# Kernel optimization log

Measured on AMD Instinct MI355X. Metric: run time of the kernel, lower is better.

The kernel has to match this reference:

```python
import jax, jax.numpy as jnp
import numpy as np

MAX_ITER = 3
DAMPING = 1e-3
HUBER_B = 0.02
LAMBDA_ICP, LAMBDA_RGB = 1.0, 1e-6
DIST_THRESH = 0.1


def pixel_grid(H, W):
    j, i = jnp.meshgrid(jnp.arange(H, dtype=jnp.float32), jnp.arange(W, dtype=jnp.float32), indexing='ij')
    return i, j  # i = x (col), j = y (row)


def compute_vertex(depth, K):
    fx, fy, cx, cy = K[0, 0], K[1, 1], K[0, 2], K[1, 2]
    H, W = depth.shape
    i, j = pixel_grid(H, W)
    return jnp.stack([(i - cx) / fx, (j - cy) / fy, jnp.ones_like(i)], -1) * depth[..., None]


def sobel(img, normalize=True):
    # replicate-padded 3x3 Sobel cross-correlation, img [H,W,C]
    p = jnp.pad(img, ((1, 1), (1, 1), (0, 0)), mode='edge')
    dx = (p[:-2, 2:] - p[:-2, :-2]) + 2.0 * (p[1:-1, 2:] - p[1:-1, :-2]) + (p[2:, 2:] - p[2:, :-2])
    dy = (p[2:, :-2] - p[:-2, :-2]) + 2.0 * (p[2:, 1:-1] - p[:-2, 1:-1]) + (p[2:, 2:] - p[:-2, 2:])
    if normalize:
        mag = jnp.sqrt(dx * dx + dy * dy + 1e-8)
        dx, dy = dx / mag, dy / mag
    return dx, dy


def compute_normal(vmap_):
    dx, dy = sobel(vmap_, normalize=False)
    n = jnp.cross(dx, dy)
    n = n / (jnp.linalg.norm(n, axis=-1, keepdims=True) + 1e-8)
    d = vmap_[..., 2]
    invalid = (d <= d.min()) | (d >= d.max())
    return jnp.where(invalid[..., None], 0.0, n)


def warp_jacobian(depth, K):
    fx, fy, cx, cy = K[0, 0], K[1, 1], K[0, 2], K[1, 2]
    H, W = depth.shape
    i, j = pixel_grid(H, W)
    x = (i - cx) / fx * depth
    y = (j - cy) / fy * depth
    invD = 1.0 / depth
    invD2 = invD * invD
    xy = x * y
    O = jnp.zeros_like(depth)
    dx_dp = jnp.stack([-invD2 * xy, 1.0 + x * x * invD2, -y * invD, invD, O, -invD2 * x], -1)
    dy_dp = jnp.stack([-1.0 - invD2 * y * y, xy * invD2, x * invD, O, invD, -invD2 * y], -1)
    return dx_dp * fx, dy_dp * fy


def bilinear(feat, u, v):
    # grid_sample(mode=bilinear, padding=border, align_corners=True) on pixel coords
    H, W, _ = feat.shape
    u = jnp.clip(u, 0.0, W - 1.0)
    v = jnp.clip(v, 0.0, H - 1.0)
    u0 = jnp.floor(u)
    v0 = jnp.floor(v)
    wu = (u - u0)[..., None]
    wv = (v - v0)[..., None]
    u0i = u0.astype(jnp.int32)
    v0i = v0.astype(jnp.int32)
    u1i = jnp.minimum(u0i + 1, W - 1)
    v1i = jnp.minimum(v0i + 1, H - 1)
    f00 = feat[v0i, u0i]
    f01 = feat[v0i, u1i]
    f10 = feat[v1i, u0i]
    f11 = feat[v1i, u1i]
    return (f00 * (1 - wu) + f01 * wu) * (1 - wv) + (f10 * (1 - wu) + f11 * wu) * wv


def project(vt, K, H, W):
    z = vt[..., 2]
    u = vt[..., 0] / z * K[0, 0] + K[0, 2]
    v = vt[..., 1] / z * K[1, 1] + K[1, 2]
    inview = (u > 0) & (u < W - 1) & (v > 0) & (v < H - 1) & (z > 0)
    return u, v, inview


def huber_weight(x, b=HUBER_B):
    rho = jnp.where(x <= b, x * x, 2.0 * b * x - b * b)
    x_safe = jnp.where(x < 1e-8, 1.0, x)
    return jnp.sqrt(rho + 1e-16) / x_safe


def skew(w):
    z = jnp.zeros((), w.dtype)
    return jnp.stack([jnp.stack([z, -w[2], w[1]]), jnp.stack([w[2], z, -w[0]]), jnp.stack([-w[1], w[0], z])])


def exp_so3(w):
    Wh = skew(w)
    th2 = jnp.maximum(jnp.sum(w * w), 1e-30)
    th = jnp.sqrt(th2)
    R = jnp.eye(3, dtype=w.dtype) + Wh * (jnp.sin(th) / th) + (Wh @ Wh) * ((1.0 - jnp.cos(th)) / th2)
    return jnp.where(th <= 1e-10, jnp.eye(3, dtype=w.dtype), R)


def icp_residuals(vertex0, vertex1, normal1, mask0, pose, K):
    H, W, _ = vertex0.shape
    R, t = pose[:3, :3], pose[:3, 3]
    v0t = vertex0 @ R.T + t  # [H,W,3]
    u, v, inview = project(v0t, K, H, W)
    v1w = bilinear(vertex1, u, v)
    n1w = bilinear(normal1, u, v)
    diff = v0t - v1w
    valid = inview & mask0 & (v1w[..., 2] > 0) & (jnp.linalg.norm(diff, axis=-1) < DIST_THRESH)
    res = jnp.where(valid, jnp.sum(n1w * diff, -1), 0.0)  # point-to-plane
    J = jnp.where(valid[..., None], jnp.concatenate([jnp.cross(v0t, n1w), n1w], -1), 0.0)  # [H,W,6]
    w = huber_weight(jnp.abs(res))
    return (w * res).reshape(-1, 1), (w[..., None] * J).reshape(-1, 1, 6)


def rgb_residuals(pose, vertex0, x0, x1, K, mask0):
    H, W, _ = x0.shape
    R, t = pose[:3, :3], pose[:3, 3]
    v0t = vertex0 @ R.T + t
    u, v, inview = project(v0t, K, H, W)
    x1w = bilinear(x1, u, v)
    invalid = (~inview) | (~mask0)
    res = jnp.where(invalid[..., None], 0.0, x1w - x0)
    return res, invalid


def inverse_update_pose(Hm, Rhs, pose):
    xi = (jnp.linalg.inv(Hm) @ Rhs).reshape(-1)
    dR = exp_so3(-xi[:3])
    dt = -dR @ xi[3:]
    R1 = dR @ pose[:3, :3]
    t1 = dR @ pose[:3, 3] + dt
    top = jnp.concatenate([R1, t1[:, None]], 1)
    return jnp.concatenate([top, pose[3:4, :]], 0)


def color_icp(pose10, depth0, depth1, x0, x1, K):
    H, W, C = x0.shape
    vertex0 = compute_vertex(depth0, K)
    normal0 = compute_normal(vertex0)  # computed as in original
    mask0 = depth0 > 0.0
    vertex1 = compute_vertex(depth1, K)
    normal1 = compute_normal(vertex1)
    # pre-computable inverse-compositional RGB jacobian: normalized image grads x warp jacobian
    gx, gy = sobel(x0, normalize=True)  # [H,W,C]
    Jx, Jy = warp_jacobian(depth0, K)  # [H,W,6]
    J_rgb_pre = gx[..., None] * Jx[:, :, None, :] + gy[..., None] * Jy[:, :, None, :]  # [H,W,C,6]
    pose = pose10
    for _ in range(MAX_ITER):
        r_icp, J_icp = icp_residuals(vertex0, vertex1, normal1, mask0, pose, K)
        JtWJ = LAMBDA_ICP * jnp.einsum('nci,ncj->ij', J_icp, J_icp)
        JtR = LAMBDA_ICP * jnp.einsum('nci,nc->i', J_icp, r_icp)
        r_rgb, invalid = rgb_residuals(pose, vertex0, x0, x1, K, mask0)
        J_rgb = jnp.where(invalid[..., None, None], 0.0, J_rgb_pre).reshape(-1, C, 6)
        JtWJ = JtWJ + LAMBDA_RGB * jnp.einsum('nci,ncj->ij', J_rgb, J_rgb)
        JtR = JtR + LAMBDA_RGB * jnp.einsum('nci,nc->i', J_rgb, r_rgb.reshape(-1, C))
        Hm = JtWJ + jnp.eye(6) * (jnp.trace(JtWJ) * DAMPING)  # Levenberg-Marquardt damping
        pose = inverse_update_pose(Hm, JtR.reshape(6, 1), pose)
    return pose


def setup_inputs() -> dict:
    key = jax.random.key(0)
    k = jax.random.split(key, 6)
    H, W = 960, 1280
    depth0 = 0.5 + 2.5 * jax.random.uniform(k[0], (H, W), jnp.float32)
    depth1 = 0.5 + 2.5 * jax.random.uniform(k[1], (H, W), jnp.float32)
    x0 = jax.random.uniform(k[2], (H, W, 3), jnp.float32)
    x1 = jax.random.uniform(k[3], (H, W, 3), jnp.float32)
    K = jnp.array([[1050.0, 0.0, (W - 1) / 2.0], [0.0, 1050.0, (H - 1) / 2.0], [0.0, 0.0, 1.0]], jnp.float32)
    w = 0.01 * jax.random.normal(k[4], (3,), jnp.float32)
    t = 0.01 * jax.random.normal(k[5], (3,), jnp.float32)
    R = exp_so3(w)
    pose10 = jnp.concatenate([jnp.concatenate([R, t[:, None]], 1),
                              jnp.array([[0.0, 0.0, 0.0, 1.0]], jnp.float32)], 0)
    return {'pose10': pose10, 'depth0': depth0, 'depth1': depth1, 'x0': x0, 'x1': x1, 'K': K}


def reference(pose10, depth0, depth1, x0, x1, K):
    return color_icp(pose10, depth0, depth1, x0, x1, K)
```

## Files before the change

kernel.cpp:

```cpp
#include <hip/hip_runtime.h>
#include <math.h>

#define HH 960
#define WW 1280
#define NPIX (HH*WW)
#define BPR (WW/256)
#define NBLK_ROW (NPIX/256)
#define NBLK_MAIN (NPIX/(256*2))
#define MM_BLOCKS 512
#define TW 258
#define PSTRIDE 28

#define WS_POSE_OFF    0
#define WS_BMIN_OFF    128
#define WS_BMAX_OFF    2176
#define WS_PARTIAL_OFF 4352
#define WS_NX_OFF      273152

__device__ __forceinline__ int clampi(int v, int lo, int hi){ return v<lo?lo:(v>hi?hi:v); }

__global__ __launch_bounds__(256) void k_pre1(const float* __restrict__ depth1,
                                              const float* __restrict__ pose_in,
                                              float* __restrict__ pose,
                                              float* __restrict__ bmin,
                                              float* __restrict__ bmax){
  int t = threadIdx.x;
  if (blockIdx.x == 0 && t < 16) pose[t] = pose_in[t];
  float mn = INFINITY, mx = 0.f;
  for (int i = blockIdx.x*256 + t; i < NPIX; i += MM_BLOCKS*256){
    float d = depth1[i];
    mn = fminf(mn, d); mx = fmaxf(mx, d);
  }
  #pragma unroll
  for (int off = 32; off; off >>= 1){
    mn = fminf(mn, __shfl_down(mn, off));
    mx = fmaxf(mx, __shfl_down(mx, off));
  }
  __shared__ float smn[4], smx[4];
  int lane = t & 63, wid = t >> 6;
  if (lane == 0){ smn[wid] = mn; smx[wid] = mx; }
  __syncthreads();
  if (t == 0){
    bmin[blockIdx.x] = fminf(fminf(smn[0], smn[1]), fminf(smn[2], smn[3]));
    bmax[blockIdx.x] = fmaxf(fmaxf(smx[0], smx[1]), fmaxf(smx[2], smx[3]));
  }
}

__global__ __launch_bounds__(256) void k_pre2(const float* __restrict__ depth1,
                                              const float* __restrict__ x1,
                                              const float* __restrict__ Kd,
                                              const float* __restrict__ bmin,
                                              const float* __restrict__ bmax,
                                              float* __restrict__ nx1){
  int t = threadIdx.x;
  float mn = fminf(bmin[t], bmin[t+256]);
  float mx = fmaxf(bmax[t], bmax[t+256]);
  #pragma unroll
  for (int off = 32; off; off >>= 1){
    mn = fminf(mn, __shfl_down(mn, off));
    mx = fmaxf(mx, __shfl_down(mx, off));
  }
  __shared__ float smn[4], smx[4];
  __shared__ float sdmn, sdmx;
  int lane = t & 63, wid = t >> 6;
  if (lane == 0){ smn[wid] = mn; smx[wid] = mx; }
  __syncthreads();
  if (t == 0){
    sdmn = fminf(fminf(smn[0], smn[1]), fminf(smn[2], smn[3]));
    sdmx = fmaxf(fmaxf(smx[0], smx[1]), fmaxf(smx[2], smx[3]));
  }
  __syncthreads();
  float dmn = sdmn, dmx = sdmx;

  int bid = blockIdx.x;
  int py = bid / BPR;
  int px = (bid % BPR)*256 + t;
  float fx = Kd[0], fy = Kd[4], cx = Kd[2], cy = Kd[5];
  float invfx = 1.f/fx, invfy = 1.f/fy;
  float vx[3][3], vy[3][3], vz[3][3];
  #pragma unroll
  for (int dr = 0; dr < 3; dr++){
    int r = clampi(py + dr - 1, 0, HH-1);
    #pragma unroll
    for (int dc = 0; dc < 3; dc++){
      int c = clampi(px + dc - 1, 0, WW-1);
      float d = depth1[r*WW + c];
      vx[dr][dc] = ((float)c - cx)*invfx*d;
      vy[dr][dc] = ((float)r - cy)*invfy*d;
      vz[dr][dc] = d;
    }
  }
  float ax_ = (vx[0][2]-vx[0][0]) + 2.f*(vx[1][2]-vx[1][0]) + (vx[2][2]-vx[2][0]);
  float ay_ = (vy[0][2]-vy[0][0]) + 2.f*(vy[1][2]-vy[1][0]) + (vy[2][2]-vy[2][0]);
  float az_ = (vz[0][2]-vz[0][0]) + 2.f*(vz[1][2]-vz[1][0]) + (vz[2][2]-vz[2][0]);
  float bx_ = (vx[2][0]-vx[0][0]) + 2.f*(vx[2][1]-vx[0][1]) + (vx[2][2]-vx[0][2]);
  float by_ = (vy[2][0]-vy[0][0]) + 2.f*(vy[2][1]-vy[0][1]) + (vy[2][2]-vy[0][2]);
  float bz_ = (vz[2][0]-vz[0][0]) + 2.f*(vz[2][1]-vz[0][1]) + (vz[2][2]-vz[0][2]);
  float nx = ay_*bz_ - az_*by_;
  float ny = az_*bx_ - ax_*bz_;
  float nz = ax_*by_ - ay_*bx_;
  float nrm = sqrtf(nx*nx + ny*ny + nz*nz) + 1e-8f;
  float rn  = __builtin_amdgcn_rcpf(nrm);
  nx *= rn; ny *= rn; nz *= rn;
  float dcen = vz[1][1];
  if (dcen <= dmn || dcen >= dmx){ nx = 0.f; ny = 0.f; nz = 0.f; }
  int idx = py*WW + px;
  const float* q = &x1[idx*3];
  float4 a; a.x = nx;   a.y = ny;   a.z = nz;   a.w = dcen;
  float4 b; b.x = q[0]; b.y = q[1]; b.z = q[2]; b.w = 0.f;
  ((float4*)nx1)[idx*2+0] = a;
  ((float4*)nx1)[idx*2+1] = b;
}

__global__ __launch_bounds__(256) void k_main(const float* __restrict__ depth0,
                                              const float* __restrict__ x0,
                                              const float* __restrict__ nx1,
                                              const float* __restrict__ Kd,
                                              const float* __restrict__ pose,
                                              float* __restrict__ partial){
  int t = threadIdx.x;
  int bid = (blockIdx.x & 7)*(NBLK_MAIN/8) + (blockIdx.x >> 3);
  int pr = bid / BPR;
  int cs = bid % BPR;
  int py0 = pr*2;
  int colbase = cs*256 - 1;
  int px = cs*256 + t;

  __shared__ float tile[4*TW*3];
  for (int s = t; s < 4*TW; s += 256){
    int r = s / TW, c = s - r*TW;
    int gr = clampi(py0 - 1 + r, 0, HH-1);
    int gc = clampi(colbase + c, 0, WW-1);
    const float* q = &x0[(gr*WW + gc)*3];
    tile[s*3+0] = q[0]; tile[s*3+1] = q[1]; tile[s*3+2] = q[2];
  }

  int idx0 = py0*WW + px;
  float d0a = depth0[idx0];
  float d0b = depth0[idx0 + WW];
  __syncthreads();

  float fx = Kd[0], fy = Kd[4], cx = Kd[2], cy = Kd[5];
  float inv_fx = 1.f/fx, inv_fy = 1.f/fy;
  float R00=pose[0], R01=pose[1], R02=pose[2],  tx=pose[3];
  float R10=pose[4], R11=pose[5], R12=pose[6],  ty=pose[7];
  float R20=pose[8], R21=pose[9], R22=pose[10], tz=pose[11];

  float acc[27];
  #pragma unroll
  for (int k = 0; k < 27; k++) acc[k] = 0.f;

  const float4* nx4 = (const float4*)nx1;

  #pragma unroll
  for (int kp = 0; kp < 2; kp++){
    int py = py0 + kp;

    float d0 = (kp == 0) ? d0a : d0b;
    bool m0 = d0 > 0.f;
    float v0x = ((float)px - cx)*inv_fx*d0;
    float v0y = ((float)py - cy)*inv_fy*d0;
    float v0z = d0;
    float X = R00*v0x + R01*v0y + R02*v0z + tx;
    float Y = R10*v0x + R11*v0y + R12*v0z + ty;
    float Z = R20*v0x + R21*v0y + R22*v0z + tz;
    float invZ = __builtin_amdgcn_rcpf(Z);
    invZ = invZ*(2.0f - Z*invZ);
    float u = X*invZ*fx + cx;
    float v = Y*invZ*fy + cy;
    bool inview = (u > 0.f) && (u < (float)(WW-1)) && (v > 0.f) && (v < (float)(HH-1)) && (Z > 0.f);

    float uc = fminf(fmaxf(u, 0.f), (float)(WW-1));
    float vc = fminf(fmaxf(v, 0.f), (float)(HH-1));
    float u0f = floorf(uc), v0f = floorf(vc);
    float wu = uc - u0f, wv = vc - v0f;
    int u0i = clampi((int)u0f, 0, WW-1);
    int v0i = clampi((int)v0f, 0, HH-1);
    int u1i = min(u0i + 1, WW-1);
    int v1i = min(v0i + 1, HH-1);
    int i00 = v0i*WW + u0i, i01 = v0i*WW + u1i, i10 = v1i*WW + u0i, i11 = v1i*WW + u1i;
    float w00 = (1.f-wu)*(1.f-wv), w01 = wu*(1.f-wv), w10 = (1.f-wu)*wv, w11 = wu*wv;

    float4 n00 = nx4[i00*2], c00 = nx4[i00*2+1];
    float4 n01 = nx4[i01*2], c01 = nx4[i01*2+1];
    float4 n10 = nx4[i10*2], c10 = nx4[i10*2+1];
    float4 n11 = nx4[i11*2], c11 = nx4[i11*2+1];

    float t0 = w00*n00.w, t1 = w01*n01.w, t2 = w10*n10.w, t3 = w11*n11.w;
    float u0c = ((float)u0i - cx)*inv_fx, u1c = ((float)u1i - cx)*inv_fx;
    float v0c = ((float)v0i - cy)*inv_fy, v1c = ((float)v1i - cy)*inv_fy;
    float s2 = (t0+t1)+(t2+t3);
    float s0 = u0c*(t0+t2) + u1c*(t1+t3);
    float s1 = v0c*(t0+t1) + v1c*(t2+t3);
    float nx = n00.x*w00 + n01.x*w01 + n10.x*w10 + n11.x*w11;
    float ny = n00.y*w00 + n01.y*w01 + n10.y*w10 + n11.y*w11;
    float nz = n00.z*w00 + n01.z*w01 + n10.z*w10 + n11.z*w11;

    float dfx = X - s0, dfy = Y - s1, dfz = Z - s2;
    bool valid = inview && m0 && (s2 > 0.f) && (dfx*dfx + dfy*dfy + dfz*dfz < 0.01f);
    float res = 0.f;
    float J[6] = {0.f,0.f,0.f,0.f,0.f,0.f};
    if (valid){
      res = nx*dfx + ny*dfy + nz*dfz;
      J[0] = Y*nz - Z*ny;
      J[1] = Z*nx - X*nz;
      J[2] = X*ny - Y*nx;
      J[3] = nx; J[4] = ny; J[5] = nz;
    }
    float axv = fabsf(res);
    float rho = (axv <= 0.02f) ? axv*axv : (0.04f*axv - 0.0004f);
    float xs  = (axv < 1e-8f) ? 1.f : axv;
    float hw  = sqrtf(rho + 1e-16f) * __builtin_amdgcn_rcpf(xs);
    float wr  = hw*res;
    float wJ[6];
    #pragma unroll
    for (int i = 0; i < 6; i++) wJ[i] = hw*J[i];
    {
      int k = 0;
      #pragma unroll
      for (int i = 0; i < 6; i++)
        #pragma unroll
        for (int j = i; j < 6; j++)
          acc[k++] += wJ[i]*wJ[j];
      #pragma unroll
      for (int i = 0; i < 6; i++) acc[21+i] += wJ[i]*wr;
    }

    if (inview && m0){
      float xw[3];
      xw[0] = c00.x*w00 + c01.x*w01 + c10.x*w10 + c11.x*w11;
      xw[1] = c00.y*w00 + c01.y*w01 + c10.y*w10 + c11.y*w11;
      xw[2] = c00.z*w00 + c01.z*w01 + c10.z*w10 + c11.z*w11;

      float ga = 0.f, gb = 0.f, gc2 = 0.f, rx = 0.f, ry = 0.f;
      #pragma unroll
      for (int ch = 0; ch < 3; ch++){
        float p00 = tile[((kp+0)*TW + (t+0))*3 + ch];
        float p01 = tile[((kp+0)*TW + (t+1))*3 + ch];
        float p02 = tile[((kp+0)*TW + (t+2))*3 + ch];
        float p10 = tile[((kp+1)*TW + (t+0))*3 + ch];
        float p11 = tile[((kp+1)*TW + (t+1))*3 + ch];
        float p12 = tile[((kp+1)*TW + (t+2))*3 + ch];
        float p20 = tile[((kp+2)*TW + (t+0))*3 + ch];
        float p21 = tile[((kp+2)*TW + (t+1))*3 + ch];
        float p22 = tile[((kp+2)*TW + (t+2))*3 + ch];
        float dx = (p02-p00) + 2.f*(p12-p10) + (p22-p20);
        float dy = (p20-p00) + 2.f*(p21-p01) + (p22-p02);
        float rinv = __builtin_amdgcn_rsqf(dx*dx + dy*dy + 1e-8f);
        float gx = dx*rinv, gy = dy*rinv;
        float rr = xw[ch] - p11;
        ga  += gx*gx; gb += gx*gy; gc2 += gy*gy;
        rx  += gx*rr; ry += gy*rr;
      }
      ga *= 1e-6f; gb *= 1e-6f; gc2 *= 1e-6f; rx *= 1e-6f; ry *= 1e-6f;

      float invD = __builtin_amdgcn_rcpf(d0), invD2 = invD*invD;
      float xy = v0x*v0y;
      float Jx[6] = { fx*(-invD2*xy), fx*(1.f + v0x*v0x*invD2), fx*(-v0y*invD), fx*invD, 0.f, fx*(-invD2*v0x) };
      float Jy[6] = { fy*(-1.f - invD2*v0y*v0y), fy*(xy*invD2), fy*(v0x*invD), 0.f, fy*invD, fy*(-invD2*v0y) };
      float P[6], Q[6];
      #pragma unroll
      for (int i = 0; i < 6; i++){ P[i] = ga*Jx[i] + gb*Jy[i]; Q[i] = gb*Jx[i] + gc2*Jy[i]; }
      int k = 0;
      #pragma unroll
      for (int i = 0; i < 6; i++)
        #pragma unroll
        for (int j = i; j < 6; j++)
          acc[k++] += Jx[j]*P[i] + Jy[j]*Q[i];
      #pragma unroll
      for (int i = 0; i < 6; i++) acc[21+i] += Jx[i]*rx + Jy[i]*ry;
    }
  }

  __shared__ float lds[108];
  int lane = t & 63;
  int wid  = t >> 6;
  #pragma unroll
  for (int k = 0; k < 27; k++){
    float vv = acc[k];
    vv += __shfl_down(vv, 32); vv += __shfl_down(vv, 16); vv += __shfl_down(vv, 8);
    vv += __shfl_down(vv, 4);  vv += __shfl_down(vv, 2);  vv += __shfl_down(vv, 1);
    if (lane == 0) lds[wid*27 + k] = vv;
  }
  __syncthreads();
  if (t < 27)
    partial[bid*PSTRIDE + t] = lds[t] + lds[27+t] + lds[54+t] + lds[81+t];
  else if (t == 27)
    partial[bid*PSTRIDE + 27] = 0.f;
}

__global__ __launch_bounds__(256) void k_solve(const float* __restrict__ partial,
                                               float* __restrict__ pose,
                                               float* __restrict__ outp){
  int t = threadIdx.x;
  double acc[PSTRIDE];
  #pragma unroll
  for (int k = 0; k < PSTRIDE; k++) acc[k] = 0.0;
  const float4* p4 = (const float4*)partial;
  for (int r = t; r < NBLK_MAIN; r += 256){
    #pragma unroll
    for (int q = 0; q < 7; q++){
      float4 vv = p4[r*7 + q];
      acc[q*4+0] += (double)vv.x;
      acc[q*4+1] += (double)vv.y;
      acc[q*4+2] += (double)vv.z;
      acc[q*4+3] += (double)vv.w;
    }
  }
  __shared__ double lds[4*PSTRIDE];
  int lane = t & 63, wid = t >> 6;
  #pragma unroll
  for (int k = 0; k < PSTRIDE; k++){
    double vv = acc[k];
    vv += __shfl_down(vv, 32); vv += __shfl_down(vv, 16); vv += __shfl_down(vv, 8);
    vv += __shfl_down(vv, 4);  vv += __shfl_down(vv, 2);  vv += __shfl_down(vv, 1);
    if (lane == 0) lds[wid*PSTRIDE + k] = vv;
  }
  __syncthreads();
  if (t == 0){
    double s[PSTRIDE];
    #pragma unroll
    for (int k = 0; k < PSTRIDE; k++)
      s[k] = lds[k] + lds[PSTRIDE+k] + lds[2*PSTRIDE+k] + lds[3*PSTRIDE+k];
    double Hm[6][6], b[6];
    {
      int k = 0;
      for (int i = 0; i < 6; i++)
        for (int j = i; j < 6; j++){ Hm[i][j] = s[k]; Hm[j][i] = s[k]; k++; }
      for (int i = 0; i < 6; i++) b[i] = s[21+i];
    }
    double tr = Hm[0][0]+Hm[1][1]+Hm[2][2]+Hm[3][3]+Hm[4][4]+Hm[5][5];
    for (int i = 0; i < 6; i++) Hm[i][i] += tr*0.001;
    double A[6][7];
    for (int i = 0; i < 6; i++){
      for (int j = 0; j < 6; j++) A[i][j] = Hm[i][j];
      A[i][6] = b[i];
    }
    for (int c = 0; c < 6; c++){
      int piv = c; double best = fabs(A[c][c]);
      for (int r = c+1; r < 6; r++){ double a = fabs(A[r][c]); if (a > best){ best = a; piv = r; } }
      if (piv != c)
        for (int j = 0; j < 7; j++){ double tv = A[c][j]; A[c][j] = A[piv][j]; A[piv][j] = tv; }
      double inv = 1.0/A[c][c];
      for (int r = 0; r < 6; r++){
        if (r == c) continue;
        double f = A[r][c]*inv;
        for (int j = c; j < 7; j++) A[r][j] -= f*A[c][j];
      }
    }
    double xi[6];
    for (int i = 0; i < 6; i++) xi[i] = A[i][6]/A[i][i];
    double wx = -xi[0], wy = -xi[1], wz = -xi[2];
    double th2 = wx*wx + wy*wy + wz*wz;
    if (th2 < 1e-30) th2 = 1e-30;
    double th = sqrt(th2);
    double dR[3][3];
    if (th <= 1e-10){
      dR[0][0]=1; dR[0][1]=0; dR[0][2]=0;
      dR[1][0]=0; dR[1][1]=1; dR[1][2]=0;
      dR[2][0]=0; dR[2][1]=0; dR[2][2]=1;
    } else {
      double sa = sin(th)/th;
      double sb = (1.0 - cos(th))/th2;
      double Wm[3][3] = {{0,-wz,wy},{wz,0,-wx},{-wy,wx,0}};
      double W2[3][3];
      for (int i = 0; i < 3; i++)
        for (int j = 0; j < 3; j++)
          W2[i][j] = Wm[i][0]*Wm[0][j] + Wm[i][1]*Wm[1][j] + Wm[i][2]*Wm[2][j];
      for (int i = 0; i < 3; i++)
        for (int j = 0; j < 3; j++)
          dR[i][j] = (i==j ? 1.0 : 0.0) + sa*Wm[i][j] + sb*W2[i][j];
    }
    double dt[3];
    for (int i = 0; i < 3; i++)
      dt[i] = -(dR[i][0]*xi[3] + dR[i][1]*xi[4] + dR[i][2]*xi[5]);
    double Ro[3][3], to[3];
    for (int i = 0; i < 3; i++){
      for (int j = 0; j < 3; j++) Ro[i][j] = (double)pose[i*4+j];
      to[i] = (double)pose[i*4+3];
    }
    double Rn[3][3], tn[3];
    for (int i = 0; i < 3; i++){
      for (int j = 0; j < 3; j++)
        Rn[i][j] = dR[i][0]*Ro[0][j] + dR[i][1]*Ro[1][j] + dR[i][2]*Ro[2][j];
      tn[i] = dR[i][0]*to[0] + dR[i][1]*to[1] + dR[i][2]*to[2] + dt[i];
    }
    float o16[16];
    for (int i = 0; i < 3; i++){
      for (int j = 0; j < 3; j++) o16[i*4+j] = (float)Rn[i][j];
      o16[i*4+3] = (float)tn[i];
    }
    o16[12] = 0.f; o16[13] = 0.f; o16[14] = 0.f; o16[15] = 1.f;
    for (int k = 0; k < 16; k++){ pose[k] = o16[k]; outp[k] = o16[k]; }
  }
}

extern "C" void kernel_launch(void* const* d_in, const int* in_sizes, int n_in,
                              void* d_out, int out_size, void* d_ws, size_t ws_size,
                              hipStream_t stream) {
  const float* pose10 = (const float*)d_in[0];
  const float* depth0 = (const float*)d_in[1];
  const float* depth1 = (const float*)d_in[2];
  const float* x0     = (const float*)d_in[3];
  const float* x1     = (const float*)d_in[4];
  const float* Kd     = (const float*)d_in[5];
  char* ws = (char*)d_ws;
  float* pose    = (float*)(ws + WS_POSE_OFF);
  float* bmin    = (float*)(ws + WS_BMIN_OFF);
  float* bmax    = (float*)(ws + WS_BMAX_OFF);
  float* partial = (float*)(ws + WS_PARTIAL_OFF);
  float* nx1     = (float*)(ws + WS_NX_OFF);
  float* outp    = (float*)d_out;

  hipLaunchKernelGGL(k_pre1, dim3(MM_BLOCKS), dim3(256), 0, stream,
                     depth1, pose10, pose, bmin, bmax);
  hipLaunchKernelGGL(k_pre2, dim3(NBLK_ROW),  dim3(256), 0, stream,
                     depth1, x1, Kd, bmin, bmax, nx1);
  for (int it = 0; it < 3; it++){
    hipLaunchKernelGGL(k_main,  dim3(NBLK_MAIN), dim3(256), 0, stream,
                       depth0, x0, nx1, Kd, pose, partial);
    hipLaunchKernelGGL(k_solve, dim3(1),         dim3(256), 0, stream, partial, pose, outp);
  }
}
```

Measured before the change: 252.5 us.

## Fuse depth min/max into normal pass and solve into main via last-block counter

Merges the two preprocessing kernels into one. Each block now writes its per-block depth min/max alongside the normals, and the invalid-normal masking moves into k_main as per-corner masks on the bilinear weights. The separate solve kernel is folded into k_main: an atomic counter elects the last finishing block, which reduces the partials and updates the pose. This removes one full read of depth1 and four kernel launches. In exchange, every k_main block redundantly reduces about 4800 min/max entries before its tile load, and a serial single-block solve now sits at the tail of each main launch.

```diff
diff --git a/kernel.cpp b/kernel.cpp
--- a/kernel.cpp
+++ b/kernel.cpp
@@ -5,74 +5,35 @@
 #define WW 1280
 #define NPIX (HH*WW)
 #define BPR (WW/256)
-#define NBLK_ROW (NPIX/256)
+#define NBLK_PRE (NPIX/256)
 #define NBLK_MAIN (NPIX/(256*2))
-#define MM_BLOCKS 512
 #define TW 258
 #define PSTRIDE 28
 
 #define WS_POSE_OFF    0
-#define WS_BMIN_OFF    128
-#define WS_BMAX_OFF    2176
-#define WS_PARTIAL_OFF 4352
-#define WS_NX_OFF      273152
+#define WS_CNT_OFF     64
+#define WS_BMIN_OFF    256
+#define WS_BMAX_OFF    19456
+#define WS_PARTIAL_OFF 38656
+#define WS_NX_OFF      307456
 
 __device__ __forceinline__ int clampi(int v, int lo, int hi){ return v<lo?lo:(v>hi?hi:v); }
 
-__global__ __launch_bounds__(256) void k_pre1(const float* __restrict__ depth1,
-                                              const float* __restrict__ pose_in,
-                                              float* __restrict__ pose,
-                                              float* __restrict__ bmin,
-                                              float* __restrict__ bmax){
+__global__ __launch_bounds__(256) void k_pre(const float* __restrict__ depth1,
+                                             const float* __restrict__ x1,
+                                             const float* __restrict__ Kd,
+                                             const float* __restrict__ pose_in,
+                                             float* __restrict__ pose,
+                                             int* __restrict__ counters,
+                                             float* __restrict__ bmin,
+                                             float* __restrict__ bmax,
+                                             float* __restrict__ nx1){
   int t = threadIdx.x;
-  if (blockIdx.x == 0 && t < 16) pose[t] = pose_in[t];
-  float mn = INFINITY, mx = 0.f;
-  for (int i = blockIdx.x*256 + t; i < NPIX; i += MM_BLOCKS*256){
-    float d = depth1[i];
-    mn = fminf(mn, d); mx = fmaxf(mx, d);
-  }
-  #pragma unroll
-  for (int off = 32; off; off >>= 1){
-    mn = fminf(mn, __shfl_down(mn, off));
-    mx = fmaxf(mx, __shfl_down(mx, off));
-  }
-  __shared__ float smn[4], smx[4];
-  int lane = t & 63, wid = t >> 6;
-  if (lane == 0){ smn[wid] = mn; smx[wid] = mx; }
-  __syncthreads();
-  if (t == 0){
-    bmin[blockIdx.x] = fminf(fminf(smn[0], smn[1]), fminf(smn[2], smn[3]));
-    bmax[blockIdx.x] = fmaxf(fmaxf(smx[0], smx[1]), fmaxf(smx[2], smx[3]));
-  }
-}
-
-__global__ __launch_bounds__(256) void k_pre2(const float* __restrict__ depth1,
-                                              const float* __restrict__ x1,
-                                              const float* __restrict__ Kd,
-                                              const float* __restrict__ bmin,
-                                              const float* __restrict__ bmax,
-                                              float* __restrict__ nx1){
-  int t = threadIdx.x;
-  float mn = fminf(bmin[t], bmin[t+256]);
-  float mx = fmaxf(bmax[t], bmax[t+256]);
-  #pragma unroll
-  for (int off = 32; off; off >>= 1){
-    mn = fminf(mn, __shfl_down(mn, off));
-    mx = fmaxf(mx, __shfl_down(mx, off));
-  }
-  __shared__ float smn[4], smx[4];
-  __shared__ float sdmn, sdmx;
-  int lane = t & 63, wid = t >> 6;
-  if (lane == 0){ smn[wid] = mn; smx[wid] = mx; }
-  __syncthreads();
-  if (t == 0){
-    sdmn = fminf(fminf(smn[0], smn[1]), fminf(smn[2], smn[3]));
-    sdmx = fmaxf(fmaxf(smx[0], smx[1]), fmaxf(smx[2], smx[3]));
-  }
-  __syncthreads();
-  float dmn = sdmn, dmx = sdmx;
-
   int bid = blockIdx.x;
+  if (bid == 0){
+    if (t < 16) pose[t] = pose_in[t];
+    if (t < 8)  counters[t] = 0;
+  }
   int py = bid / BPR;
   int px = (bid % BPR)*256 + t;
   float fx = Kd[0], fy = Kd[4], cx = Kd[2], cy = Kd[5];
@@ -103,22 +64,62 @@
   float rn  = __builtin_amdgcn_rcpf(nrm);
   nx *= rn; ny *= rn; nz *= rn;
   float dcen = vz[1][1];
-  if (dcen <= dmn || dcen >= dmx){ nx = 0.f; ny = 0.f; nz = 0.f; }
   int idx = py*WW + px;
   const float* q = &x1[idx*3];
   float4 a; a.x = nx;   a.y = ny;   a.z = nz;   a.w = dcen;
   float4 b; b.x = q[0]; b.y = q[1]; b.z = q[2]; b.w = 0.f;
   ((float4*)nx1)[idx*2+0] = a;
   ((float4*)nx1)[idx*2+1] = b;
+
+  float mn = dcen, mx = dcen;
+  #pragma unroll
+  for (int off = 32; off; off >>= 1){
+    mn = fminf(mn, __shfl_down(mn, off));
+    mx = fmaxf(mx, __shfl_down(mx, off));
+  }
+  __shared__ float smn[4], smx[4];
+  int lane = t & 63, wid = t >> 6;
+  if (lane == 0){ smn[wid] = mn; smx[wid] = mx; }
+  __syncthreads();
+  if (t == 0){
+    bmin[bid] = fminf(fminf(smn[0], smn[1]), fminf(smn[2], smn[3]));
+    bmax[bid] = fmaxf(fmaxf(smx[0], smx[1]), fmaxf(smx[2], smx[3]));
+  }
 }
 
 __global__ __launch_bounds__(256) void k_main(const float* __restrict__ depth0,
                                               const float* __restrict__ x0,
                                               const float* __restrict__ nx1,
                                               const float* __restrict__ Kd,
-                                              const float* __restrict__ pose,
-                                              float* __restrict__ partial){
+                                              float* __restrict__ pose,
+                                              const float* __restrict__ bmin,
+                                              const float* __restrict__ bmax,
+                                              float* __restrict__ partial,
+                                              int* __restrict__ counter,
+                                              float* __restrict__ outp){
   int t = threadIdx.x;
+  int lane = t & 63, wid = t >> 6;
+  __shared__ float lds[108];
+  __shared__ float sdmn, sdmx;
+
+  {
+    float mn = INFINITY, mx = 0.f;
+    for (int i = t; i < NBLK_PRE; i += 256){
+      mn = fminf(mn, bmin[i]); mx = fmaxf(mx, bmax[i]);
+    }
+    #pragma unroll
+    for (int off = 32; off; off >>= 1){
+      mn = fminf(mn, __shfl_down(mn, off));
+      mx = fmaxf(mx, __shfl_down(mx, off));
+    }
+    if (lane == 0){ lds[wid] = mn; lds[8+wid] = mx; }
+    __syncthreads();
+    if (t == 0){
+      sdmn = fminf(fminf(lds[0], lds[1]), fminf(lds[2], lds[3]));
+      sdmx = fmaxf(fmaxf(lds[8], lds[9]), fmaxf(lds[10], lds[11]));
+    }
+  }
+
   int bid = (blockIdx.x & 7)*(NBLK_MAIN/8) + (blockIdx.x >> 3);
   int pr = bid / BPR;
   int cs = bid % BPR;
@@ -134,11 +135,11 @@
     const float* q = &x0[(gr*WW + gc)*3];
     tile[s*3+0] = q[0]; tile[s*3+1] = q[1]; tile[s*3+2] = q[2];
   }
-
   int idx0 = py0*WW + px;
   float d0a = depth0[idx0];
   float d0b = depth0[idx0 + WW];
   __syncthreads();
+  float dmn = sdmn, dmx = sdmx;
 
   float fx = Kd[0], fy = Kd[4], cx = Kd[2], cy = Kd[5];
   float inv_fx = 1.f/fx, inv_fy = 1.f/fy;
@@ -155,7 +156,6 @@
   #pragma unroll
   for (int kp = 0; kp < 2; kp++){
     int py = py0 + kp;
-
     float d0 = (kp == 0) ? d0a : d0b;
     bool m0 = d0 > 0.f;
     float v0x = ((float)px - cx)*inv_fx*d0;
@@ -186,15 +186,21 @@
     float4 n10 = nx4[i10*2], c10 = nx4[i10*2+1];
     float4 n11 = nx4[i11*2], c11 = nx4[i11*2+1];
 
+    float m00f = (n00.w > dmn && n00.w < dmx) ? 1.f : 0.f;
+    float m01f = (n01.w > dmn && n01.w < dmx) ? 1.f : 0.f;
+    float m10f = (n10.w > dmn && n10.w < dmx) ? 1.f : 0.f;
+    float m11f = (n11.w > dmn && n11.w < dmx) ? 1.f : 0.f;
+    float wn00 = w00*m00f, wn01 = w01*m01f, wn10 = w10*m10f, wn11 = w11*m11f;
+
     float t0 = w00*n00.w, t1 = w01*n01.w, t2 = w10*n10.w, t3 = w11*n11.w;
     float u0c = ((float)u0i - cx)*inv_fx, u1c = ((float)u1i - cx)*inv_fx;
     float v0c = ((float)v0i - cy)*inv_fy, v1c = ((float)v1i - cy)*inv_fy;
     float s2 = (t0+t1)+(t2+t3);
     float s0 = u0c*(t0+t2) + u1c*(t1+t3);
     float s1 = v0c*(t0+t1) + v1c*(t2+t3);
-    float nx = n00.x*w00 + n01.x*w01 + n10.x*w10 + n11.x*w11;
-    float ny = n00.y*w00 + n01.y*w01 + n10.y*w10 + n11.y*w11;
-    float nz = n00.z*w00 + n01.z*w01 + n10.z*w10 + n11.z*w11;
+    float nx = n00.x*wn00 + n01.x*wn01 + n10.x*wn10 + n11.x*wn11;
+    float ny = n00.y*wn00 + n01.y*wn01 + n10.y*wn10 + n11.y*wn11;
+    float nz = n00.z*wn00 + n01.z*wn01 + n10.z*wn10 + n11.z*wn11;
 
     float dfx = X - s0, dfy = Y - s1, dfz = Z - s2;
     bool valid = inview && m0 && (s2 > 0.f) && (dfx*dfx + dfy*dfy + dfz*dfz < 0.01f);
@@ -272,9 +278,6 @@
     }
   }
 
-  __shared__ float lds[108];
-  int lane = t & 63;
-  int wid  = t >> 6;
   #pragma unroll
   for (int k = 0; k < 27; k++){
     float vv = acc[k];
@@ -287,54 +290,56 @@
     partial[bid*PSTRIDE + t] = lds[t] + lds[27+t] + lds[54+t] + lds[81+t];
   else if (t == 27)
     partial[bid*PSTRIDE + 27] = 0.f;
-}
-
-__global__ __launch_bounds__(256) void k_solve(const float* __restrict__ partial,
-                                               float* __restrict__ pose,
-                                               float* __restrict__ outp){
-  int t = threadIdx.x;
-  double acc[PSTRIDE];
-  #pragma unroll
-  for (int k = 0; k < PSTRIDE; k++) acc[k] = 0.0;
+
+  __shared__ int slast;
+  __threadfence();
+  __syncthreads();
+  if (t == 0) slast = (atomicAdd(counter, 1) == NBLK_MAIN - 1) ? 1 : 0;
+  __syncthreads();
+  if (!slast) return;
+  __threadfence();
+
+  __shared__ double lds2[4*PSTRIDE];
+  double acc2[PSTRIDE];
+  #pragma unroll
+  for (int k = 0; k < PSTRIDE; k++) acc2[k] = 0.0;
   const float4* p4 = (const float4*)partial;
   for (int r = t; r < NBLK_MAIN; r += 256){
     #pragma unroll
     for (int q = 0; q < 7; q++){
       float4 vv = p4[r*7 + q];
-      acc[q*4+0] += (double)vv.x;
-      acc[q*4+1] += (double)vv.y;
-      acc[q*4+2] += (double)vv.z;
-      acc[q*4+3] += (double)vv.w;
-    }
-  }
-  __shared__ double lds[4*PSTRIDE];
-  int lane = t & 63, wid = t >> 6;
+      acc2[q*4+0] += (double)vv.x;
+      acc2[q*4+1] += (double)vv.y;
+      acc2[q*4+2] += (double)vv.z;
+      acc2[q*4+3] += (double)vv.w;
+    }
+  }
   #pragma unroll
   for (int k = 0; k < PSTRIDE; k++){
-    double vv = acc[k];
+    double vv = acc2[k];
     vv += __shfl_down(vv, 32); vv += __shfl_down(vv, 16); vv += __shfl_down(vv, 8);
     vv += __shfl_down(vv, 4);  vv += __shfl_down(vv, 2);  vv += __shfl_down(vv, 1);
-    if (lane == 0) lds[wid*PSTRIDE + k] = vv;
+    if (lane == 0) lds2[wid*PSTRIDE + k] = vv;
   }
   __syncthreads();
   if (t == 0){
     double s[PSTRIDE];
     #pragma unroll
     for (int k = 0; k < PSTRIDE; k++)
-      s[k] = lds[k] + lds[PSTRIDE+k] + lds[2*PSTRIDE+k] + lds[3*PSTRIDE+k];
-    double Hm[6][6], b[6];
+      s[k] = lds2[k] + lds2[PSTRIDE+k] + lds2[2*PSTRIDE+k] + lds2[3*PSTRIDE+k];
+    double Hm[6][6], bv[6];
     {
       int k = 0;
       for (int i = 0; i < 6; i++)
         for (int j = i; j < 6; j++){ Hm[i][j] = s[k]; Hm[j][i] = s[k]; k++; }
-      for (int i = 0; i < 6; i++) b[i] = s[21+i];
+      for (int i = 0; i < 6; i++) bv[i] = s[21+i];
     }
     double tr = Hm[0][0]+Hm[1][1]+Hm[2][2]+Hm[3][3]+Hm[4][4]+Hm[5][5];
     for (int i = 0; i < 6; i++) Hm[i][i] += tr*0.001;
     double A[6][7];
     for (int i = 0; i < 6; i++){
       for (int j = 0; j < 6; j++) A[i][j] = Hm[i][j];
-      A[i][6] = b[i];
+      A[i][6] = bv[i];
     }
     for (int c = 0; c < 6; c++){
       int piv = c; double best = fabs(A[c][c]);
@@ -406,19 +411,18 @@
   const float* Kd     = (const float*)d_in[5];
   char* ws = (char*)d_ws;
   float* pose    = (float*)(ws + WS_POSE_OFF);
+  int*   counters= (int*)(ws + WS_CNT_OFF);
   float* bmin    = (float*)(ws + WS_BMIN_OFF);
   float* bmax    = (float*)(ws + WS_BMAX_OFF);
   float* partial = (float*)(ws + WS_PARTIAL_OFF);
   float* nx1     = (float*)(ws + WS_NX_OFF);
   float* outp    = (float*)d_out;
 
-  hipLaunchKernelGGL(k_pre1, dim3(MM_BLOCKS), dim3(256), 0, stream,
-                     depth1, pose10, pose, bmin, bmax);
-  hipLaunchKernelGGL(k_pre2, dim3(NBLK_ROW),  dim3(256), 0, stream,
-                     depth1, x1, Kd, bmin, bmax, nx1);
+  hipLaunchKernelGGL(k_pre, dim3(NBLK_PRE), dim3(256), 0, stream,
+                     depth1, x1, Kd, pose10, pose, counters, bmin, bmax, nx1);
   for (int it = 0; it < 3; it++){
-    hipLaunchKernelGGL(k_main,  dim3(NBLK_MAIN), dim3(256), 0, stream,
-                       depth0, x0, nx1, Kd, pose, partial);
-    hipLaunchKernelGGL(k_solve, dim3(1),         dim3(256), 0, stream, partial, pose, outp);
+    hipLaunchKernelGGL(k_main, dim3(NBLK_MAIN), dim3(256), 0, stream,
+                       depth0, x0, nx1, Kd, pose, bmin, bmax, partial,
+                       counters + it, outp);
   }
 }
```

Result: slower. 700.5 us (+177.4%).
